# Kernel optimization log

Hardware: AMD Instinct MI355X
Metric: run time of the kernel (lower is better)

## Reference

```python
import jax, jax.numpy as jnp
import numpy as np

P_FACTOR = 3.0
EPS = 1e-12  # torch F.normalize eps


def _l2norm(x):
    # torch.nn.functional.normalize(x, dim=1): x / max(||x||_2, eps)
    n = jnp.sqrt(jnp.sum(x * x, axis=1, keepdims=True))
    return x / jnp.maximum(n, EPS)


def setup_inputs() -> dict:
    key = jax.random.key(0)
    k1, k2, k3, k4, k5 = jax.random.split(key, 5)
    B, N, D_IN, D_RED, C = 8192, 16384, 1024, 512, 28
    return {
        "features": jax.random.normal(k1, (B, D_IN), dtype=jnp.float32),
        "ex_features": jax.random.normal(k2, (N, D_IN), dtype=jnp.float32),
        "g_w": jax.random.normal(k3, (D_RED, D_IN), dtype=jnp.float32) * 0.02,
        "g_b": jax.random.normal(k4, (D_RED,), dtype=jnp.float32) * 0.02,
        "ex_classes": jax.random.uniform(k5, (N, C), dtype=jnp.float32),
    }


def reference(features, ex_features, g_w, g_b, ex_classes):
    # g: Linear(input_dim -> dim_reduce)
    f = features @ g_w.T + g_b          # [B, D_red]
    ef = ex_features @ g_w.T + g_b      # [N, D_red]
    # cosine similarity
    s = _l2norm(f) @ _l2norm(ef).T      # [B, N]
    # power-sign activation: |s|^p * sign(s)
    a = jnp.power(jnp.abs(s), P_FACTOR) * jnp.sign(s)
    echo = a @ ex_classes               # [B, C]
    b = jnp.clip(jnp.sum(ex_classes, axis=0), 1.0, None)
    echo = jnp.clip(echo / b, 0.0, 1.0)
    return echo
```

## Files before the change

kernel.cpp:

```cpp
#include <hip/hip_runtime.h>
#include <stdint.h>

typedef __attribute__((ext_vector_type(4))) float f32x4;
typedef __attribute__((ext_vector_type(8))) short s16x8;

#define MFMA16(A, B, C) __builtin_amdgcn_mfma_f32_16x16x32_bf16(A, B, C, 0, 0, 0)
#define WAIT_VM(N) asm volatile("s_waitcnt vmcnt(" #N ")" ::: "memory")
#define WAIT_LGKM() asm volatile("s_waitcnt lgkmcnt(0)" ::: "memory")
#define BAR() __builtin_amdgcn_s_barrier()
#define SCHED_FENCE() __builtin_amdgcn_sched_barrier(0)
#define SP1() __builtin_amdgcn_s_setprio(1)
#define SP0() __builtin_amdgcn_s_setprio(0)

__device__ __forceinline__ unsigned short f2bf(float x) {
  union { float f; unsigned u; } v; v.f = x;
  return (unsigned short)((v.u + 0x7fffu + ((v.u >> 16) & 1u)) >> 16);
}

__global__ void k_cast_bf16(const float* __restrict__ in, unsigned short* __restrict__ out, int n4) {
  int i = blockIdx.x * blockDim.x + threadIdx.x;
  const int stride = gridDim.x * blockDim.x;
  for (; i < n4; i += stride) {
    const float4 v = ((const float4*)in)[i];
    ushort4 o;
    o.x = f2bf(v.x); o.y = f2bf(v.y); o.z = f2bf(v.z); o.w = f2bf(v.w);
    ((ushort4*)out)[i] = o;
  }
}

__global__ void k_excT(const float* __restrict__ exc, unsigned short* __restrict__ excT,
                       float* __restrict__ bvec) {
  const int c = blockIdx.x;
  const int tid = threadIdx.x;
  float sum = 0.f;
  for (int j = tid; j < 16384; j += 256) {
    const float v = (c < 28) ? exc[(size_t)j * 28 + c] : 0.f;
    excT[(size_t)c * 16384 + j] = f2bf(v);
    sum += v;
  }
  #pragma unroll
  for (int o = 32; o; o >>= 1) sum += __shfl_down(sum, o, 64);
  __shared__ float wsum[4];
  if ((tid & 63) == 0) wsum[tid >> 6] = sum;
  __syncthreads();
  if (tid == 0 && c < 28) bvec[c] = fmaxf(wsum[0] + wsum[1] + wsum[2] + wsum[3], 1.0f);
}

__device__ __forceinline__ void stage_a(const unsigned short* __restrict__ src, int ld,
                                        unsigned short* smem, int dsoff, int w, int offsrc) {
  #pragma unroll
  for (int c = 0; c < 4; ++c)
    __builtin_amdgcn_global_load_lds(
        (const __attribute__((address_space(1))) unsigned int*)(src + offsrc + c * 64 * ld),
        (__attribute__((address_space(3))) unsigned int*)(smem + dsoff + c * 4096 + w * 512),
        16, 0, 0);
}
__device__ __forceinline__ void stage_b(const unsigned short* __restrict__ src, int ld,
                                        unsigned short* smem, int dsoff, int w, int offsrc) {
  #pragma unroll
  for (int c = 0; c < 2; ++c)
    __builtin_amdgcn_global_load_lds(
        (const __attribute__((address_space(1))) unsigned int*)(src + offsrc + c * 64 * ld),
        (__attribute__((address_space(3))) unsigned int*)(smem + dsoff + c * 4096 + w * 512),
        16, 0, 0);
}

__device__ __forceinline__ void mma_step_p(const unsigned short* smem, int ao, int bo,
                                           int wr, int wc, int r, int q, f32x4 acc[8][2]) {
  const int rx = r & 7;
  #pragma unroll
  for (int ks = 0; ks < 2; ++ks) {
    const int sb = ((ks * 4 + q) ^ rx) << 3;
    s16x8 bf[2];
    #pragma unroll
    for (int j = 0; j < 2; ++j)
      bf[j] = *(const s16x8*)(smem + bo + (wc * 32 + j * 16 + r) * 64 + sb);
    #pragma unroll
    for (int i = 0; i < 8; ++i) {
      const s16x8 af = *(const s16x8*)(smem + ao + (wr * 128 + i * 16 + r) * 64 + sb);
      #pragma unroll
      for (int j = 0; j < 2; ++j)
        acc[i][j] = MFMA16(af, bf[j], acc[i][j]);
    }
  }
}

#define PA0 0
#define PB0 16384
#define PA1 24576
#define PB1 40960

__global__ __launch_bounds__(512, 2) void k_proj(const unsigned short* __restrict__ featbf,
                                                 const unsigned short* __restrict__ exbf,
                                                 const unsigned short* __restrict__ gwbf,
                                                 const float* __restrict__ gb,
                                                 float* __restrict__ fall) {
  __shared__ __align__(16) unsigned short smem[49152];
  const int tid = threadIdx.x, w = tid >> 6, lane = tid & 63;
  const int wr = w >> 2, wc = w & 3, r = lane & 15, q = lane >> 4;
  const int offsrc = (w * 8 + (lane >> 3)) * 1024 + (((lane & 7) ^ (lane >> 3)) << 3);
  const int m0 = blockIdx.x * 256;
  const int n0 = blockIdx.y * 128;
  const unsigned short* Asrc = (m0 < 8192) ? (featbf + (size_t)m0 * 1024)
                                           : (exbf + (size_t)(m0 - 8192) * 1024);
  const unsigned short* Bsrc = gwbf + (size_t)n0 * 1024;
  f32x4 acc[8][2];
  #pragma unroll
  for (int i = 0; i < 8; ++i)
    #pragma unroll
    for (int j = 0; j < 2; ++j) acc[i][j] = {0.f, 0.f, 0.f, 0.f};

  stage_a(Asrc, 1024, smem, PA0, w, offsrc);
  stage_b(Bsrc, 1024, smem, PB0, w, offsrc);
  for (int t = 0; t < 15; ++t) {
    const int na = ((t + 1) & 1) ? PA1 : PA0, nbb = ((t + 1) & 1) ? PB1 : PB0;
    stage_a(Asrc + (t + 1) * 64, 1024, smem, na, w, offsrc);
    stage_b(Bsrc + (t + 1) * 64, 1024, smem, nbb, w, offsrc);
    WAIT_VM(6);
    BAR();
    mma_step_p(smem, (t & 1) ? PA1 : PA0, (t & 1) ? PB1 : PB0, wr, wc, r, q, acc);
    WAIT_LGKM();
    BAR();
  }
  WAIT_VM(0);
  BAR();
  mma_step_p(smem, PA1, PB1, wr, wc, r, q, acc);

  #pragma unroll
  for (int j = 0; j < 2; ++j) {
    const int col = n0 + wc * 32 + j * 16 + r;
    const float bias = gb[col];
    #pragma unroll
    for (int i = 0; i < 8; ++i) {
      const int row0 = m0 + wr * 128 + i * 16 + q * 4;
      #pragma unroll
      for (int t = 0; t < 4; ++t)
        fall[(size_t)(row0 + t) * 512 + col] = acc[i][j][t] + bias;
    }
  }
}

__global__ __launch_bounds__(256) void k_norm(const float* __restrict__ fall,
                                              unsigned short* __restrict__ fn) {
  const int row = blockIdx.x * 4 + (threadIdx.x >> 6);
  const int lane = threadIdx.x & 63;
  const float4* p = (const float4*)(fall + (size_t)row * 512) + lane * 2;
  const float4 v0 = p[0], v1 = p[1];
  float ss = v0.x * v0.x + v0.y * v0.y + v0.z * v0.z + v0.w * v0.w
           + v1.x * v1.x + v1.y * v1.y + v1.z * v1.z + v1.w * v1.w;
  #pragma unroll
  for (int o = 32; o; o >>= 1) ss += __shfl_xor(ss, o, 64);
  const float sc = 1.0f / fmaxf(sqrtf(ss), 1e-12f);
  ushort4 o0, o1;
  o0.x = f2bf(v0.x * sc); o0.y = f2bf(v0.y * sc); o0.z = f2bf(v0.z * sc); o0.w = f2bf(v0.w * sc);
  o1.x = f2bf(v1.x * sc); o1.y = f2bf(v1.y * sc); o1.z = f2bf(v1.z * sc); o1.w = f2bf(v1.w * sc);
  ushort4* qo = (ushort4*)(fn + (size_t)row * 512) + lane * 2;
  qo[0] = o0; qo[1] = o1;
}

#define BUF 16384
#define EXLo 32768
#define ALo 40960

__device__ __forceinline__ void stage_p(const unsigned short* __restrict__ src,
                                        unsigned short* smem, int dsoff, int tid) {
  const unsigned short* g = src + (size_t)(tid >> 2) * 512 + (tid & 3) * 8;
  __builtin_amdgcn_global_load_lds(
      (const __attribute__((address_space(1))) unsigned int*)g,
      (__attribute__((address_space(3))) unsigned int*)(smem + dsoff + tid * 8), 16, 0, 0);
}

__device__ __forceinline__ void stage_exc(const unsigned short* __restrict__ excTg, int c0,
                                          unsigned short* smem, int tid) {
  const int row = tid >> 5, b = tid & 31;
  const int sb = ((b & 24) | ((b ^ (row & 7)) & 7)) << 3;
  const unsigned short* g = excTg + (size_t)row * 16384 + c0 + sb;
  __builtin_amdgcn_global_load_lds(
      (const __attribute__((address_space(1))) unsigned int*)g,
      (__attribute__((address_space(3))) unsigned int*)(smem + EXLo + tid * 8), 16, 0, 0);
  __builtin_amdgcn_global_load_lds(
      (const __attribute__((address_space(1))) unsigned int*)(g + 16 * 16384),
      (__attribute__((address_space(3))) unsigned int*)(smem + EXLo + 4096 + tid * 8), 16, 0, 0);
}

__device__ __forceinline__ void ktile32(const unsigned short* smem, int bufR,
                                        int wr, int wc, int r, int q, f32x4 acc[2][2][4][2]) {
  const int koff = q * 8;
  const unsigned short* Bb = smem + bufR + 8192 + (wc * 32 + r) * 32 + koff;
  s16x8 bf[2][2];
  #pragma unroll
  for (int nh = 0; nh < 2; ++nh)
    #pragma unroll
    for (int fj = 0; fj < 2; ++fj)
      bf[nh][fj] = *(const s16x8*)(Bb + (nh * 128 + fj * 16) * 32);
  #pragma unroll
  for (int MH = 0; MH < 2; ++MH) {
    const unsigned short* Ab = smem + bufR + (MH * 128 + wr * 64 + r) * 32 + koff;
    #pragma unroll
    for (int fi = 0; fi < 4; ++fi) {
      const s16x8 af = *(const s16x8*)(Ab + fi * 512);
      #pragma unroll
      for (int nh = 0; nh < 2; ++nh)
        #pragma unroll
        for (int fj = 0; fj < 2; ++fj)
          acc[MH][nh][fi][fj] = MFMA16(af, bf[nh][fj], acc[MH][nh][fi][fj]);
    }
  }
}

__global__ __launch_bounds__(512, 2) void k_fused(const unsigned short* __restrict__ fnall,
                                                  const unsigned short* __restrict__ excT,
                                                  float* __restrict__ partial) {
  __shared__ __align__(16) unsigned short smem[73728];
  const int tid = threadIdx.x, w = tid >> 6, lane = tid & 63;
  const int wr = w >> 2, wc = w & 3, r = lane & 15, q = lane >> 4, rx = r & 7;
  const int r0 = blockIdx.x * 256;
  const int nchunk = blockIdx.y;
  const unsigned short* Abase = fnall + (size_t)r0 * 512;
  const unsigned short* Ebase = fnall + (size_t)8192 * 512;
  unsigned short* aLb = smem + ALo;

  f32x4 acc[2][2][4][2];
  f32x4 eacc[2][2];
  #pragma unroll
  for (int a = 0; a < 2; ++a)
    #pragma unroll
    for (int b = 0; b < 2; ++b) eacc[a][b] = {0.f, 0.f, 0.f, 0.f};

  {
    const unsigned short* Bp = Ebase + (size_t)(nchunk * 4) * 256 * 512;
    stage_p(Bp, smem, 8192, tid);
    stage_p(Bp + 128 * 512, smem, 12288, tid);
    stage_p(Abase, smem, 0, tid);
    stage_p(Abase + 128 * 512, smem, 4096, tid);
  }

  for (int jt = 0; jt < 4; ++jt) {
    const int c0 = (nchunk * 4 + jt) * 256;
    const unsigned short* Bsrc = Ebase + (size_t)c0 * 512;
    #pragma unroll
    for (int a = 0; a < 2; ++a)
      #pragma unroll
      for (int b = 0; b < 2; ++b)
        #pragma unroll
        for (int fi = 0; fi < 4; ++fi)
          #pragma unroll
          for (int fj = 0; fj < 2; ++fj) acc[a][b][fi][fj] = {0.f, 0.f, 0.f, 0.f};

    for (int tk = 0; tk < 16; ++tk) {
      const int bufR = (tk & 1) * BUF, bufW = bufR ^ BUF;
      SCHED_FENCE(); WAIT_LGKM(); WAIT_VM(0); BAR(); SCHED_FENCE();
      if (tk < 15) {
        const unsigned short* An = Abase + (tk + 1) * 32;
        const unsigned short* Bn = Bsrc + (tk + 1) * 32;
        stage_p(Bn, smem, bufW + 8192, tid);
        stage_p(Bn + 128 * 512, smem, bufW + 12288, tid);
        stage_p(An, smem, bufW + 0, tid);
        stage_p(An + 128 * 512, smem, bufW + 4096, tid);
      } else {
        stage_exc(excT, c0, smem, tid);
        if (jt < 3) {
          const unsigned short* Bn = Ebase + (size_t)(c0 + 256) * 512;
          stage_p(Bn, smem, bufW + 8192, tid);
          stage_p(Bn + 128 * 512, smem, bufW + 12288, tid);
          stage_p(Abase, smem, bufW + 0, tid);
          stage_p(Abase + 128 * 512, smem, bufW + 4096, tid);
        }
      }
      SP1(); ktile32(smem, bufR, wr, wc, r, q, acc); SP0();
    }

    SCHED_FENCE(); WAIT_LGKM();
    if (jt < 3) { WAIT_VM(4); } else { WAIT_VM(0); }
    BAR(); SCHED_FENCE();
    #pragma unroll
    for (int h = 0; h < 2; ++h) {
      #pragma unroll
      for (int nh = 0; nh < 2; ++nh)
        #pragma unroll
        for (int fi = 0; fi < 4; ++fi)
          #pragma unroll
          for (int fj = 0; fj < 2; ++fj) {
            const int colc = nh * 128 + wc * 32 + fj * 16 + r;
            const int cb = colc >> 3, cl = colc & 7;
            #pragma unroll
            for (int t2 = 0; t2 < 4; ++t2) {
              const int row = wr * 64 + fi * 16 + q * 4 + t2;
              const float v = acc[h][nh][fi][fj][t2];
              aLb[row * 256 + ((((cb & 24) | ((cb ^ (row & 7)) & 7)) << 3) | cl)] = f2bf(v * v * v);
            }
          }
      SCHED_FENCE(); WAIT_LGKM(); BAR(); SCHED_FENCE();
      {
        const int rE = w * 16 + r;
        const int re8 = rE & 7;
        #pragma unroll
        for (int kc = 0; kc < 8; ++kc) {
          const int kb = kc * 4 + q;
          const s16x8 af = *(const s16x8*)(aLb + rE * 256 + (((kb & 24) | ((kb ^ re8) & 7)) << 3));
          #pragma unroll
          for (int nj = 0; nj < 2; ++nj) {
            const s16x8 bfr = *(const s16x8*)(smem + EXLo + (nj * 16 + r) * 256 +
                                              (((kb & 24) | ((kb ^ rx) & 7)) << 3));
            eacc[h][nj] = MFMA16(af, bfr, eacc[h][nj]);
          }
        }
      }
      SCHED_FENCE(); WAIT_LGKM(); BAR(); SCHED_FENCE();
    }
  }

  #pragma unroll
  for (int h = 0; h < 2; ++h)
    #pragma unroll
    for (int nj = 0; nj < 2; ++nj) {
      const int rb = r0 + h * 128 + w * 16 + q * 4;
      const int cls = nj * 16 + r;
      #pragma unroll
      for (int t = 0; t < 4; ++t)
        partial[((size_t)nchunk * 8192 + rb + t) * 32 + cls] = eacc[h][nj][t];
    }
}

__global__ void k_reduce(const float* __restrict__ partial, const float* __restrict__ bvec,
                         float* __restrict__ out) {
  const int idx = blockIdx.x * 256 + threadIdx.x;
  const int row = idx / 28, c = idx - row * 28;
  float s = 0.f;
  #pragma unroll
  for (int nc = 0; nc < 16; ++nc) s += partial[((size_t)nc * 8192 + row) * 32 + c];
  out[idx] = fminf(fmaxf(s / bvec[c], 0.f), 1.f);
}

extern "C" void kernel_launch(void* const* d_in, const int* in_sizes, int n_in,
                              void* d_out, int out_size, void* d_ws, size_t ws_size,
                              hipStream_t stream) {
  const float* features    = (const float*)d_in[0];
  const float* ex_features = (const float*)d_in[1];
  const float* g_w         = (const float*)d_in[2];
  const float* g_b         = (const float*)d_in[3];
  const float* ex_classes  = (const float*)d_in[4];
  float* out = (float*)d_out;
  char* ws = (char*)d_ws;

  unsigned short* featbf = (unsigned short*)(ws + 0);
  unsigned short* exbf   = (unsigned short*)(ws + 16777216);
  unsigned short* fnall  = (unsigned short*)(ws + 0);
  float* fall            = (float*)(ws + 50331648);
  float* partial         = (float*)(ws + 50331648);
  unsigned short* gwbf   = (unsigned short*)(ws + 100663296);
  unsigned short* excT   = (unsigned short*)(ws + 101711872);
  float* bvec            = (float*)(ws + 102760448);

  k_cast_bf16<<<2048, 256, 0, stream>>>(features, featbf, 8192 * 1024 / 4);
  k_cast_bf16<<<2048, 256, 0, stream>>>(ex_features, exbf, 16384 * 1024 / 4);
  k_cast_bf16<<<512, 256, 0, stream>>>(g_w, gwbf, 512 * 1024 / 4);
  k_excT<<<32, 256, 0, stream>>>(ex_classes, excT, bvec);
  k_proj<<<dim3(96, 4), 512, 0, stream>>>(featbf, exbf, gwbf, g_b, fall);
  k_norm<<<6144, 256, 0, stream>>>(fall, fnall);
  k_fused<<<dim3(32, 16), 512, 0, stream>>>(fnall, excT, partial);
  k_reduce<<<896, 256, 0, stream>>>(partial, bvec, out);
}
```

Measured before the change: 250.2 us.

## Double fused kernel to 1024 threads per block with swizzled LDS staging

Block size grows from 512 to 1024 threads (16 waves), so each wave holds a 64x64 accumulator tile instead of 128x64 and issues fewer MFMAs per k-step. Staging now uses one load per thread per operand, and an XOR swizzle on the k-offset is added to cut LDS bank conflicts on fragment reads. In the epilogue, the echo matmul is split across waves by class half, and only the waves owning each row half write the cubed activations. The aim is more latency hiding and lower register pressure. The cost is a larger block with the same 144 KB of LDS, and launch_bounds(1024,4) cannot actually fit four blocks per CU.

```diff
diff --git a/kernel.cpp b/kernel.cpp
--- a/kernel.cpp
+++ b/kernel.cpp
@@ -162,11 +162,10 @@
 #define EXLo 32768
 #define ALo 40960
 
-__device__ __forceinline__ void stage_p(const unsigned short* __restrict__ src,
-                                        unsigned short* smem, int dsoff, int tid) {
-  const unsigned short* g = src + (size_t)(tid >> 2) * 512 + (tid & 3) * 8;
+__device__ __forceinline__ void stage_t(const unsigned short* __restrict__ src,
+                                        unsigned short* smem, int dsoff, int tid, int soff) {
   __builtin_amdgcn_global_load_lds(
-      (const __attribute__((address_space(1))) unsigned int*)g,
+      (const __attribute__((address_space(1))) unsigned int*)(src + soff),
       (__attribute__((address_space(3))) unsigned int*)(smem + dsoff + tid * 8), 16, 0, 0);
 }
 
@@ -174,136 +173,109 @@
                                           unsigned short* smem, int tid) {
   const int row = tid >> 5, b = tid & 31;
   const int sb = ((b & 24) | ((b ^ (row & 7)) & 7)) << 3;
-  const unsigned short* g = excTg + (size_t)row * 16384 + c0 + sb;
   __builtin_amdgcn_global_load_lds(
-      (const __attribute__((address_space(1))) unsigned int*)g,
+      (const __attribute__((address_space(1))) unsigned int*)(excTg + (size_t)row * 16384 + c0 + sb),
       (__attribute__((address_space(3))) unsigned int*)(smem + EXLo + tid * 8), 16, 0, 0);
-  __builtin_amdgcn_global_load_lds(
-      (const __attribute__((address_space(1))) unsigned int*)(g + 16 * 16384),
-      (__attribute__((address_space(3))) unsigned int*)(smem + EXLo + 4096 + tid * 8), 16, 0, 0);
-}
-
-__device__ __forceinline__ void ktile32(const unsigned short* smem, int bufR,
-                                        int wr, int wc, int r, int q, f32x4 acc[2][2][4][2]) {
-  const int koff = q * 8;
-  const unsigned short* Bb = smem + bufR + 8192 + (wc * 32 + r) * 32 + koff;
-  s16x8 bf[2][2];
-  #pragma unroll
-  for (int nh = 0; nh < 2; ++nh)
-    #pragma unroll
-    for (int fj = 0; fj < 2; ++fj)
-      bf[nh][fj] = *(const s16x8*)(Bb + (nh * 128 + fj * 16) * 32);
-  #pragma unroll
-  for (int MH = 0; MH < 2; ++MH) {
-    const unsigned short* Ab = smem + bufR + (MH * 128 + wr * 64 + r) * 32 + koff;
-    #pragma unroll
-    for (int fi = 0; fi < 4; ++fi) {
-      const s16x8 af = *(const s16x8*)(Ab + fi * 512);
-      #pragma unroll
-      for (int nh = 0; nh < 2; ++nh)
-        #pragma unroll
-        for (int fj = 0; fj < 2; ++fj)
-          acc[MH][nh][fi][fj] = MFMA16(af, bf[nh][fj], acc[MH][nh][fi][fj]);
-    }
-  }
-}
-
-__global__ __launch_bounds__(512, 2) void k_fused(const unsigned short* __restrict__ fnall,
-                                                  const unsigned short* __restrict__ excT,
-                                                  float* __restrict__ partial) {
+}
+
+__device__ __forceinline__ void ktile(const unsigned short* smem, int bufR,
+                                      int wr, int wc, int r, int koff, f32x4 acc[4][4]) {
+  const unsigned short* Bb = smem + bufR + 8192 + (wc * 64 + r) * 32 + koff;
+  s16x8 bf[4];
+  #pragma unroll
+  for (int fj = 0; fj < 4; ++fj)
+    bf[fj] = *(const s16x8*)(Bb + fj * 512);
+  #pragma unroll
+  for (int fi = 0; fi < 4; ++fi) {
+    const s16x8 af = *(const s16x8*)(smem + bufR + (wr * 64 + fi * 16 + r) * 32 + koff);
+    #pragma unroll
+    for (int fj = 0; fj < 4; ++fj)
+      acc[fi][fj] = MFMA16(af, bf[fj], acc[fi][fj]);
+  }
+}
+
+__global__ __launch_bounds__(1024, 4) void k_fused(const unsigned short* __restrict__ fnall,
+                                                   const unsigned short* __restrict__ excT,
+                                                   float* __restrict__ partial) {
   __shared__ __align__(16) unsigned short smem[73728];
   const int tid = threadIdx.x, w = tid >> 6, lane = tid & 63;
   const int wr = w >> 2, wc = w & 3, r = lane & 15, q = lane >> 4, rx = r & 7;
+  const int koff = (q ^ ((r >> 1) & 3)) << 3;
+  const int soff = (tid >> 2) * 512 + (((tid & 3) ^ ((tid >> 3) & 3)) << 3);
   const int r0 = blockIdx.x * 256;
   const int nchunk = blockIdx.y;
   const unsigned short* Abase = fnall + (size_t)r0 * 512;
   const unsigned short* Ebase = fnall + (size_t)8192 * 512;
   unsigned short* aLb = smem + ALo;
 
-  f32x4 acc[2][2][4][2];
-  f32x4 eacc[2][2];
-  #pragma unroll
-  for (int a = 0; a < 2; ++a)
-    #pragma unroll
-    for (int b = 0; b < 2; ++b) eacc[a][b] = {0.f, 0.f, 0.f, 0.f};
+  f32x4 acc[4][4];
+  f32x4 eacc[2];
+  eacc[0] = {0.f, 0.f, 0.f, 0.f};
+  eacc[1] = {0.f, 0.f, 0.f, 0.f};
 
   {
     const unsigned short* Bp = Ebase + (size_t)(nchunk * 4) * 256 * 512;
-    stage_p(Bp, smem, 8192, tid);
-    stage_p(Bp + 128 * 512, smem, 12288, tid);
-    stage_p(Abase, smem, 0, tid);
-    stage_p(Abase + 128 * 512, smem, 4096, tid);
+    stage_t(Bp, smem, 8192, tid, soff);
+    stage_t(Abase, smem, 0, tid, soff);
   }
 
   for (int jt = 0; jt < 4; ++jt) {
     const int c0 = (nchunk * 4 + jt) * 256;
     const unsigned short* Bsrc = Ebase + (size_t)c0 * 512;
     #pragma unroll
-    for (int a = 0; a < 2; ++a)
+    for (int fi = 0; fi < 4; ++fi)
       #pragma unroll
-      for (int b = 0; b < 2; ++b)
-        #pragma unroll
-        for (int fi = 0; fi < 4; ++fi)
-          #pragma unroll
-          for (int fj = 0; fj < 2; ++fj) acc[a][b][fi][fj] = {0.f, 0.f, 0.f, 0.f};
+      for (int fj = 0; fj < 4; ++fj) acc[fi][fj] = {0.f, 0.f, 0.f, 0.f};
 
     for (int tk = 0; tk < 16; ++tk) {
       const int bufR = (tk & 1) * BUF, bufW = bufR ^ BUF;
       SCHED_FENCE(); WAIT_LGKM(); WAIT_VM(0); BAR(); SCHED_FENCE();
       if (tk < 15) {
-        const unsigned short* An = Abase + (tk + 1) * 32;
-        const unsigned short* Bn = Bsrc + (tk + 1) * 32;
-        stage_p(Bn, smem, bufW + 8192, tid);
-        stage_p(Bn + 128 * 512, smem, bufW + 12288, tid);
-        stage_p(An, smem, bufW + 0, tid);
-        stage_p(An + 128 * 512, smem, bufW + 4096, tid);
+        stage_t(Bsrc + (tk + 1) * 32, smem, bufW + 8192, tid, soff);
+        stage_t(Abase + (tk + 1) * 32, smem, bufW + 0, tid, soff);
       } else {
         stage_exc(excT, c0, smem, tid);
         if (jt < 3) {
-          const unsigned short* Bn = Ebase + (size_t)(c0 + 256) * 512;
-          stage_p(Bn, smem, bufW + 8192, tid);
-          stage_p(Bn + 128 * 512, smem, bufW + 12288, tid);
-          stage_p(Abase, smem, bufW + 0, tid);
-          stage_p(Abase + 128 * 512, smem, bufW + 4096, tid);
+          stage_t(Ebase + (size_t)(c0 + 256) * 512, smem, bufW + 8192, tid, soff);
+          stage_t(Abase, smem, bufW + 0, tid, soff);
         }
       }
-      SP1(); ktile32(smem, bufR, wr, wc, r, q, acc); SP0();
+      SP1(); ktile(smem, bufR, wr, wc, r, koff, acc); SP0();
     }
 
     SCHED_FENCE(); WAIT_LGKM();
-    if (jt < 3) { WAIT_VM(4); } else { WAIT_VM(0); }
+    if (jt < 3) { WAIT_VM(2); } else { WAIT_VM(0); }
     BAR(); SCHED_FENCE();
+    const int hmine = wr >> 1;
     #pragma unroll
     for (int h = 0; h < 2; ++h) {
-      #pragma unroll
-      for (int nh = 0; nh < 2; ++nh)
+      if (hmine == h) {
         #pragma unroll
         for (int fi = 0; fi < 4; ++fi)
           #pragma unroll
-          for (int fj = 0; fj < 2; ++fj) {
-            const int colc = nh * 128 + wc * 32 + fj * 16 + r;
-            const int cb = colc >> 3, cl = colc & 7;
+          for (int fj = 0; fj < 4; ++fj) {
+            const int col = wc * 64 + fj * 16 + r;
+            const int cb = col >> 3, cl = col & 7;
             #pragma unroll
             for (int t2 = 0; t2 < 4; ++t2) {
-              const int row = wr * 64 + fi * 16 + q * 4 + t2;
-              const float v = acc[h][nh][fi][fj][t2];
-              aLb[row * 256 + ((((cb & 24) | ((cb ^ (row & 7)) & 7)) << 3) | cl)] = f2bf(v * v * v);
+              const int rowl = (wr & 1) * 64 + fi * 16 + q * 4 + t2;
+              const float v = acc[fi][fj][t2];
+              aLb[rowl * 256 + ((((cb & 24) | ((cb ^ (rowl & 7)) & 7)) << 3) | cl)] = f2bf(v * v * v);
             }
           }
+      }
       SCHED_FENCE(); WAIT_LGKM(); BAR(); SCHED_FENCE();
       {
-        const int rE = w * 16 + r;
+        const int rE = (w & 7) * 16 + r;
         const int re8 = rE & 7;
+        const int njo = (w >> 3) * 16;
         #pragma unroll
         for (int kc = 0; kc < 8; ++kc) {
           const int kb = kc * 4 + q;
           const s16x8 af = *(const s16x8*)(aLb + rE * 256 + (((kb & 24) | ((kb ^ re8) & 7)) << 3));
-          #pragma unroll
-          for (int nj = 0; nj < 2; ++nj) {
-            const s16x8 bfr = *(const s16x8*)(smem + EXLo + (nj * 16 + r) * 256 +
-                                              (((kb & 24) | ((kb ^ rx) & 7)) << 3));
-            eacc[h][nj] = MFMA16(af, bfr, eacc[h][nj]);
-          }
+          const s16x8 bfr = *(const s16x8*)(smem + EXLo + (njo + r) * 256 +
+                                            (((kb & 24) | ((kb ^ rx) & 7)) << 3));
+          eacc[h] = MFMA16(af, bfr, eacc[h]);
         }
       }
       SCHED_FENCE(); WAIT_LGKM(); BAR(); SCHED_FENCE();
@@ -311,15 +283,13 @@
   }
 
   #pragma unroll
-  for (int h = 0; h < 2; ++h)
-    #pragma unroll
-    for (int nj = 0; nj < 2; ++nj) {
-      const int rb = r0 + h * 128 + w * 16 + q * 4;
-      const int cls = nj * 16 + r;
-      #pragma unroll
-      for (int t = 0; t < 4; ++t)
-        partial[((size_t)nchunk * 8192 + rb + t) * 32 + cls] = eacc[h][nj][t];
-    }
+  for (int h = 0; h < 2; ++h) {
+    const int rb = r0 + h * 128 + (w & 7) * 16 + q * 4;
+    const int cls = (w >> 3) * 16 + r;
+    #pragma unroll
+    for (int t = 0; t < 4; ++t)
+      partial[((size_t)nchunk * 8192 + rb + t) * 32 + cls] = eacc[h][t];
+  }
 }
 
 __global__ void k_reduce(const float* __restrict__ partial, const float* __restrict__ bvec,
@@ -358,6 +328,6 @@
   k_excT<<<32, 256, 0, stream>>>(ex_classes, excT, bvec);
   k_proj<<<dim3(96, 4), 512, 0, stream>>>(featbf, exbf, gwbf, g_b, fall);
   k_norm<<<6144, 256, 0, stream>>>(fall, fnall);
-  k_fused<<<dim3(32, 16), 512, 0, stream>>>(fnall, excT, partial);
+  k_fused<<<dim3(32, 16), 1024, 0, stream>>>(fnall, excT, partial);
   k_reduce<<<896, 256, 0, stream>>>(partial, bvec, out);
 }
```

Result: slower. 557.0 us (+122.6%).
